# Kernel optimization log

Measured on AMD Instinct MI355X. Metric: run time of the kernel, lower is better.

## Reference

```python
import jax, jax.numpy as jnp
import numpy as np

N = 8192          # number of nodes
DIN = 512         # in_features
DOUT = 256        # out_features
P_EDGE = 0.004    # ~32 avg degree
NEG_INF = -9e15   # matches the torch module's -9000000000000000.0 mask value


def setup_inputs() -> dict:
    key = jax.random.key(0)
    ks = jax.random.split(key, 7)
    x = jax.random.normal(ks[0], (N, DIN), dtype=jnp.float32)
    # binary adjacency, Bernoulli(P_EDGE)
    adj = (jax.random.uniform(ks[1], (N, N)) < P_EDGE).astype(jnp.float32)
    W1 = jax.random.normal(ks[2], (DIN, DOUT), dtype=jnp.float32) * 0.05
    b1 = jnp.zeros((DOUT,), dtype=jnp.float32)
    a1_w = jax.random.normal(ks[3], (DOUT,), dtype=jnp.float32) * 0.05
    a1_b = jnp.zeros((), dtype=jnp.float32)
    a2_w = jax.random.normal(ks[4], (DOUT,), dtype=jnp.float32) * 0.05
    a2_b = jnp.zeros((), dtype=jnp.float32)
    return {"x": x, "adj": adj, "W1": W1, "b1": b1,
            "a1_w": a1_w, "a1_b": a1_b, "a2_w": a2_w, "a2_b": a2_b}


def reference(x, adj, W1, b1, a1_w, a1_b, a2_w, a2_b):
    # h = linear1(elu(x))                       [n, DOUT]
    h = jnp.matmul(jax.nn.elu(x), W1) + b1
    # per-node scalar scores g1 (source/col) and g2 (dest/row)
    g1 = h @ a1_w + a1_b                       # [n]
    g2 = h @ a2_w + a2_b                       # [n]
    # kron trick collapses to: scores[i,j] = adj[i,j] * (g2[i] + g1[j])
    scores = adj * (g2[:, None] + g1[None, :])  # [n, n]
    e = jax.nn.leaky_relu(scores, negative_slope=0.2)
    attention = jax.nn.softmax(jnp.where(adj > 0, e, NEG_INF), axis=1)
    # untied=False path: weighted aggregation of h (dropout p=0 is identity)
    return attention @ h
```

## Files before the change

### kernel.cpp

```cpp
#include <hip/hip_runtime.h>
#include <hip/hip_bf16.h>
#include <cstdint>
#include <cstddef>

#define N_NODES 8192
#define DIN 512
#define DOUT 256
#define CAP 128
#define GEMM_BLKS 512
#define SCAN_BLKS 2048

typedef short bf16x8 __attribute__((ext_vector_type(8)));
typedef float f32x4 __attribute__((ext_vector_type(4)));
typedef unsigned int u32x4 __attribute__((ext_vector_type(4)));

__device__ __forceinline__ float bf2f(unsigned short u) {
    union { unsigned int ui; float f; } v; v.ui = ((unsigned int)u) << 16; return v.f;
}
__device__ __forceinline__ unsigned short f2bf(float f) {
    union { float f; unsigned int u; } v; v.f = f;
    unsigned int u = v.u;
    return (unsigned short)((u + 0x7fffu + ((u >> 16) & 1u)) >> 16);
}
__device__ __forceinline__ float elu1(float v) { return v > 0.f ? v : (expf(v) - 1.f); }

__global__ __launch_bounds__(256) void convw_kernel(
    const float* __restrict__ W1, unsigned short* __restrict__ wb)
{
    const int n = blockIdx.x;
    const int k = threadIdx.x * 2;
    unsigned short a = f2bf(W1[(size_t)k * DOUT + n]);
    unsigned short b = f2bf(W1[(size_t)(k + 1) * DOUT + n]);
    *(unsigned int*)(wb + (size_t)n * DIN + k) = (unsigned int)a | ((unsigned int)b << 16);
}

__global__ __launch_bounds__(256) void fused_kernel(
    const float* __restrict__ x, const unsigned short* __restrict__ wb,
    const float* __restrict__ b1,
    const float* __restrict__ a1w, const float* __restrict__ a1b,
    const float* __restrict__ a2w, const float* __restrict__ a2b,
    unsigned short* __restrict__ h, float* __restrict__ g1, float* __restrict__ g2,
    const float* __restrict__ adj, int* __restrict__ ecnt, int* __restrict__ ecols)
{
    const int tid = threadIdx.x;

    if (blockIdx.x < GEMM_BLKS) {
        const int wave = tid >> 6, lane = tid & 63;
        const int quad = lane >> 4, r16 = lane & 15;
        const int m0 = blockIdx.x * 16;
        const int n0 = wave * 64;

        f32x4 acc[4] = {{0.f,0.f,0.f,0.f},{0.f,0.f,0.f,0.f},{0.f,0.f,0.f,0.f},{0.f,0.f,0.f,0.f}};
        const float* xrow = x + (size_t)(m0 + r16) * DIN;

        for (int k0 = 0; k0 < DIN; k0 += 32) {
            const int kb = k0 + quad * 8;
            float4 f0 = *(const float4*)(xrow + kb);
            float4 f1 = *(const float4*)(xrow + kb + 4);
            bf16x8 A;
            A[0] = (short)f2bf(elu1(f0.x)); A[1] = (short)f2bf(elu1(f0.y));
            A[2] = (short)f2bf(elu1(f0.z)); A[3] = (short)f2bf(elu1(f0.w));
            A[4] = (short)f2bf(elu1(f1.x)); A[5] = (short)f2bf(elu1(f1.y));
            A[6] = (short)f2bf(elu1(f1.z)); A[7] = (short)f2bf(elu1(f1.w));
            bf16x8 B[4];
            #pragma unroll
            for (int s = 0; s < 4; ++s)
                B[s] = *(const bf16x8*)(wb + (size_t)(n0 + s * 16 + r16) * DIN + kb);
            #pragma unroll
            for (int ni = 0; ni < 4; ++ni)
                acc[ni] = __builtin_amdgcn_mfma_f32_16x16x32_bf16(A, B[ni], acc[ni], 0, 0, 0);
        }

        float p1[4] = {0.f, 0.f, 0.f, 0.f};
        float p2[4] = {0.f, 0.f, 0.f, 0.f};
        #pragma unroll
        for (int ni = 0; ni < 4; ++ni) {
            const int col = n0 + ni * 16 + r16;
            const float bias = b1[col];
            const float w1c = a1w[col], w2c = a2w[col];
            #pragma unroll
            for (int rr = 0; rr < 4; ++rr) {
                float val = acc[ni][rr] + bias;
                h[(size_t)(m0 + quad * 4 + rr) * DOUT + col] = f2bf(val);
                p1[rr] += val * w1c;
                p2[rr] += val * w2c;
            }
        }
        #pragma unroll
        for (int off = 1; off < 16; off <<= 1) {
            #pragma unroll
            for (int rr = 0; rr < 4; ++rr) {
                p1[rr] += __shfl_xor(p1[rr], off, 64);
                p2[rr] += __shfl_xor(p2[rr], off, 64);
            }
        }
        __shared__ float sg1[16][4];
        __shared__ float sg2[16][4];
        if (r16 == 0) {
            #pragma unroll
            for (int rr = 0; rr < 4; ++rr) {
                sg1[quad * 4 + rr][wave] = p1[rr];
                sg2[quad * 4 + rr][wave] = p2[rr];
            }
        }
        __syncthreads();
        if (tid < 16) {
            float t1 = sg1[tid][0] + sg1[tid][1] + sg1[tid][2] + sg1[tid][3];
            float t2 = sg2[tid][0] + sg2[tid][1] + sg2[tid][2] + sg2[tid][3];
            g1[m0 + tid] = t1 + a1b[0];
            g2[m0 + tid] = t2 + a2b[0];
        }
        return;
    }

    __shared__ int eidx[4][CAP];
    __shared__ int wcnt[4];

    const int w    = tid >> 6;
    const int lane = tid & 63;
    const int i    = (blockIdx.x - GEMM_BLKS) * 4 + w;

    if (lane == 0) wcnt[w] = 0;

    const float* arow = adj + (size_t)i * N_NODES;

    #pragma unroll 1
    for (int g = 0; g < 4; ++g) {
        u32x4 raws[8];
        #pragma unroll
        for (int c = 0; c < 8; ++c)
            raws[c] = __builtin_nontemporal_load(
                (const u32x4*)(arow + (g * 8 + c) * 256 + lane * 4));
        #pragma unroll
        for (int c = 0; c < 8; ++c) {
            u32x4 raw = raws[c];
            if (raw.x | raw.y | raw.z | raw.w) {
                unsigned int wv[4] = {raw.x, raw.y, raw.z, raw.w};
                #pragma unroll
                for (int q = 0; q < 4; ++q) {
                    if (wv[q]) {
                        int j = (g * 8 + c) * 256 + lane * 4 + q;
                        int pos = atomicAdd(&wcnt[w], 1);
                        if (pos < CAP) eidx[w][pos] = j;
                    }
                }
            }
        }
    }

    int K = wcnt[w];
    if (K > CAP) K = CAP;
    if (lane == 0) ecnt[i] = K;
    for (int k = lane; k < K; k += 64)
        ecols[(size_t)i * CAP + k] = eidx[w][k];
}

__global__ __launch_bounds__(256) void agg2_kernel(
    const int* __restrict__ ecnt, const int* __restrict__ ecols,
    const unsigned short* __restrict__ h,
    const float* __restrict__ g1, const float* __restrict__ g2,
    float* __restrict__ out)
{
    __shared__ float evs[4][CAP];
    __shared__ int   jls[4][CAP];

    const int tid  = threadIdx.x;
    const int w    = tid >> 6;
    const int lane = tid & 63;
    const int i    = blockIdx.x * 4 + w;

    int K = ecnt[i];
    if (K > CAP) K = CAP;
    const float g2i = g2[i];

    if (K == 0) {
        f32x4 acc = {0.f, 0.f, 0.f, 0.f};
        for (int j = 0; j < N_NODES; ++j) {
            ushort4 hv = *(const ushort4*)(h + (size_t)j * DOUT + lane * 4);
            acc[0] += bf2f(hv.x); acc[1] += bf2f(hv.y);
            acc[2] += bf2f(hv.z); acc[3] += bf2f(hv.w);
        }
        const float sc = 1.f / (float)N_NODES;
        float4 o = {acc[0] * sc, acc[1] * sc, acc[2] * sc, acc[3] * sc};
        *(float4*)(out + (size_t)i * DOUT + lane * 4) = o;
        return;
    }

    float e0 = -1e30f, e1 = -1e30f;
    int   j0 = 0,      j1 = 0;
    if (lane < K) {
        j0 = ecols[(size_t)i * CAP + lane];
        float s = g2i + g1[j0];
        e0 = s > 0.f ? s : 0.2f * s;
    }
    if (lane + 64 < K) {
        j1 = ecols[(size_t)i * CAP + lane + 64];
        float s = g2i + g1[j1];
        e1 = s > 0.f ? s : 0.2f * s;
    }
    float m = fmaxf(e0, e1);
    #pragma unroll
    for (int off = 32; off > 0; off >>= 1) m = fmaxf(m, __shfl_xor(m, off, 64));

    float p0 = expf(e0 - m);
    float p1 = expf(e1 - m);
    float ssum = p0 + p1;
    #pragma unroll
    for (int off = 32; off > 0; off >>= 1) ssum += __shfl_xor(ssum, off, 64);
    const float inv = 1.f / ssum;

    evs[w][lane] = p0;      jls[w][lane] = j0;
    evs[w][lane + 64] = p1; jls[w][lane + 64] = j1;

    const unsigned short* hp = h + lane * 4;
    f32x4 accA = {0.f, 0.f, 0.f, 0.f};
    f32x4 accB = {0.f, 0.f, 0.f, 0.f};
    int k = 0;
    for (; k + 4 <= K; k += 4) {
        float q0 = evs[w][k],   q1 = evs[w][k+1], q2 = evs[w][k+2], q3 = evs[w][k+3];
        int   i0 = jls[w][k],   i1 = jls[w][k+1], i2 = jls[w][k+2], i3 = jls[w][k+3];
        ushort4 h0 = *(const ushort4*)(hp + (size_t)i0 * DOUT);
        ushort4 h1 = *(const ushort4*)(hp + (size_t)i1 * DOUT);
        ushort4 h2 = *(const ushort4*)(hp + (size_t)i2 * DOUT);
        ushort4 h3 = *(const ushort4*)(hp + (size_t)i3 * DOUT);
        accA[0] += q0 * bf2f(h0.x); accA[1] += q0 * bf2f(h0.y);
        accA[2] += q0 * bf2f(h0.z); accA[3] += q0 * bf2f(h0.w);
        accB[0] += q1 * bf2f(h1.x); accB[1] += q1 * bf2f(h1.y);
        accB[2] += q1 * bf2f(h1.z); accB[3] += q1 * bf2f(h1.w);
        accA[0] += q2 * bf2f(h2.x); accA[1] += q2 * bf2f(h2.y);
        accA[2] += q2 * bf2f(h2.z); accA[3] += q2 * bf2f(h2.w);
        accB[0] += q3 * bf2f(h3.x); accB[1] += q3 * bf2f(h3.y);
        accB[2] += q3 * bf2f(h3.z); accB[3] += q3 * bf2f(h3.w);
    }
    for (; k < K; ++k) {
        float q = evs[w][k];
        ushort4 hv = *(const ushort4*)(hp + (size_t)jls[w][k] * DOUT);
        accA[0] += q * bf2f(hv.x); accA[1] += q * bf2f(hv.y);
        accA[2] += q * bf2f(hv.z); accA[3] += q * bf2f(hv.w);
    }
    float4 o = {(accA[0] + accB[0]) * inv, (accA[1] + accB[1]) * inv,
                (accA[2] + accB[2]) * inv, (accA[3] + accB[3]) * inv};
    *(float4*)(out + (size_t)i * DOUT + lane * 4) = o;
}

extern "C" void kernel_launch(void* const* d_in, const int* in_sizes, int n_in,
                              void* d_out, int out_size, void* d_ws, size_t ws_size,
                              hipStream_t stream) {
    const float* x   = (const float*)d_in[0];
    const float* adj = (const float*)d_in[1];
    const float* W1  = (const float*)d_in[2];
    const float* b1  = (const float*)d_in[3];
    const float* a1w = (const float*)d_in[4];
    const float* a1b = (const float*)d_in[5];
    const float* a2w = (const float*)d_in[6];
    const float* a2b = (const float*)d_in[7];

    char* w = (char*)d_ws;
    float* g1 = (float*)w;                     w += (size_t)N_NODES * 4;
    float* g2 = (float*)w;                     w += (size_t)N_NODES * 4;
    unsigned short* h  = (unsigned short*)w;   w += (size_t)N_NODES * DOUT * 2;
    unsigned short* wb = (unsigned short*)w;   w += (size_t)DOUT * DIN * 2;
    int* ecnt = (int*)w;                       w += (size_t)N_NODES * 4;
    int* ecols = (int*)w;
    float* out = (float*)d_out;

    hipLaunchKernelGGL(convw_kernel, dim3(256), dim3(256), 0, stream, W1, wb);
    hipLaunchKernelGGL(fused_kernel, dim3(GEMM_BLKS + SCAN_BLKS), dim3(256), 0, stream,
                       x, wb, b1, a1w, a1b, a2w, a2b, h, g1, g2, adj, ecnt, ecols);
    hipLaunchKernelGGL(agg2_kernel, dim3(2048), dim3(256), 0, stream, ecnt, ecols, h, g1, g2, out);
}
```

Measured before the change: 390.6 us.

## Fuse aggregation into scan kernel using a global done-counter spin wait

Merges the aggregation kernel into the fused GEMM+scan kernel. Scan blocks keep their edge lists in shared memory and spin on a global atomic counter until all GEMM blocks have published h, g1 and g2, then compute the softmax and aggregation directly. This removes the ecnt/ecols round-trip through global memory and one kernel launch. In exchange it relies on the GEMM blocks being scheduled before the scan blocks can starve them. It also has a bounded spin that, if it times out, silently reads incomplete data.

```diff
diff --git a/kernel.cpp b/kernel.cpp
--- a/kernel.cpp
+++ b/kernel.cpp
@@ -25,13 +25,14 @@
 __device__ __forceinline__ float elu1(float v) { return v > 0.f ? v : (expf(v) - 1.f); }
 
 __global__ __launch_bounds__(256) void convw_kernel(
-    const float* __restrict__ W1, unsigned short* __restrict__ wb)
+    const float* __restrict__ W1, unsigned short* __restrict__ wb, int* __restrict__ done)
 {
     const int n = blockIdx.x;
     const int k = threadIdx.x * 2;
     unsigned short a = f2bf(W1[(size_t)k * DOUT + n]);
     unsigned short b = f2bf(W1[(size_t)(k + 1) * DOUT + n]);
     *(unsigned int*)(wb + (size_t)n * DIN + k) = (unsigned int)a | ((unsigned int)b << 16);
+    if (blockIdx.x == 0 && threadIdx.x == 0) *done = 0;
 }
 
 __global__ __launch_bounds__(256) void fused_kernel(
@@ -40,7 +41,8 @@
     const float* __restrict__ a1w, const float* __restrict__ a1b,
     const float* __restrict__ a2w, const float* __restrict__ a2b,
     unsigned short* __restrict__ h, float* __restrict__ g1, float* __restrict__ g2,
-    const float* __restrict__ adj, int* __restrict__ ecnt, int* __restrict__ ecols)
+    const float* __restrict__ adj, int* __restrict__ done,
+    float* __restrict__ out)
 {
     const int tid = threadIdx.x;
 
@@ -110,11 +112,15 @@
             g1[m0 + tid] = t1 + a1b[0];
             g2[m0 + tid] = t2 + a2b[0];
         }
+        __syncthreads();
+        if (tid == 0)
+            __hip_atomic_fetch_add(done, 1, __ATOMIC_RELEASE, __HIP_MEMORY_SCOPE_AGENT);
         return;
     }
 
-    __shared__ int eidx[4][CAP];
-    __shared__ int wcnt[4];
+    __shared__ int   eidx[4][CAP];
+    __shared__ float evs[4][CAP];
+    __shared__ int   wcnt[4];
 
     const int w    = tid >> 6;
     const int lane = tid & 63;
@@ -148,28 +154,17 @@
         }
     }
 
+    __syncthreads();
+    if (tid == 0) {
+        int it = 0;
+        while (__hip_atomic_load(done, __ATOMIC_ACQUIRE, __HIP_MEMORY_SCOPE_AGENT) < GEMM_BLKS) {
+            if (++it > (1 << 18)) break;
+            __builtin_amdgcn_s_sleep(2);
+        }
+    }
+    __syncthreads();
+
     int K = wcnt[w];
-    if (K > CAP) K = CAP;
-    if (lane == 0) ecnt[i] = K;
-    for (int k = lane; k < K; k += 64)
-        ecols[(size_t)i * CAP + k] = eidx[w][k];
-}
-
-__global__ __launch_bounds__(256) void agg2_kernel(
-    const int* __restrict__ ecnt, const int* __restrict__ ecols,
-    const unsigned short* __restrict__ h,
-    const float* __restrict__ g1, const float* __restrict__ g2,
-    float* __restrict__ out)
-{
-    __shared__ float evs[4][CAP];
-    __shared__ int   jls[4][CAP];
-
-    const int tid  = threadIdx.x;
-    const int w    = tid >> 6;
-    const int lane = tid & 63;
-    const int i    = blockIdx.x * 4 + w;
-
-    int K = ecnt[i];
     if (K > CAP) K = CAP;
     const float g2i = g2[i];
 
@@ -189,12 +184,12 @@
     float e0 = -1e30f, e1 = -1e30f;
     int   j0 = 0,      j1 = 0;
     if (lane < K) {
-        j0 = ecols[(size_t)i * CAP + lane];
+        j0 = eidx[w][lane];
         float s = g2i + g1[j0];
         e0 = s > 0.f ? s : 0.2f * s;
     }
     if (lane + 64 < K) {
-        j1 = ecols[(size_t)i * CAP + lane + 64];
+        j1 = eidx[w][lane + 64];
         float s = g2i + g1[j1];
         e1 = s > 0.f ? s : 0.2f * s;
     }
@@ -209,8 +204,8 @@
     for (int off = 32; off > 0; off >>= 1) ssum += __shfl_xor(ssum, off, 64);
     const float inv = 1.f / ssum;
 
-    evs[w][lane] = p0;      jls[w][lane] = j0;
-    evs[w][lane + 64] = p1; jls[w][lane + 64] = j1;
+    evs[w][lane] = p0;
+    evs[w][lane + 64] = p1;
 
     const unsigned short* hp = h + lane * 4;
     f32x4 accA = {0.f, 0.f, 0.f, 0.f};
@@ -218,7 +213,7 @@
     int k = 0;
     for (; k + 4 <= K; k += 4) {
         float q0 = evs[w][k],   q1 = evs[w][k+1], q2 = evs[w][k+2], q3 = evs[w][k+3];
-        int   i0 = jls[w][k],   i1 = jls[w][k+1], i2 = jls[w][k+2], i3 = jls[w][k+3];
+        int   i0 = eidx[w][k],  i1 = eidx[w][k+1], i2 = eidx[w][k+2], i3 = eidx[w][k+3];
         ushort4 h0 = *(const ushort4*)(hp + (size_t)i0 * DOUT);
         ushort4 h1 = *(const ushort4*)(hp + (size_t)i1 * DOUT);
         ushort4 h2 = *(const ushort4*)(hp + (size_t)i2 * DOUT);
@@ -234,7 +229,7 @@
     }
     for (; k < K; ++k) {
         float q = evs[w][k];
-        ushort4 hv = *(const ushort4*)(hp + (size_t)jls[w][k] * DOUT);
+        ushort4 hv = *(const ushort4*)(hp + (size_t)eidx[w][k] * DOUT);
         accA[0] += q * bf2f(hv.x); accA[1] += q * bf2f(hv.y);
         accA[2] += q * bf2f(hv.z); accA[3] += q * bf2f(hv.w);
     }
@@ -260,12 +255,10 @@
     float* g2 = (float*)w;                     w += (size_t)N_NODES * 4;
     unsigned short* h  = (unsigned short*)w;   w += (size_t)N_NODES * DOUT * 2;
     unsigned short* wb = (unsigned short*)w;   w += (size_t)DOUT * DIN * 2;
-    int* ecnt = (int*)w;                       w += (size_t)N_NODES * 4;
-    int* ecols = (int*)w;
+    int* done = (int*)w;
     float* out = (float*)d_out;
 
-    hipLaunchKernelGGL(convw_kernel, dim3(256), dim3(256), 0, stream, W1, wb);
+    hipLaunchKernelGGL(convw_kernel, dim3(256), dim3(256), 0, stream, W1, wb, done);
     hipLaunchKernelGGL(fused_kernel, dim3(GEMM_BLKS + SCAN_BLKS), dim3(256), 0, stream,
-                       x, wb, b1, a1w, a1b, a2w, a2b, h, g1, g2, adj, ecnt, ecols);
-    hipLaunchKernelGGL(agg2_kernel, dim3(2048), dim3(256), 0, stream, ecnt, ecols, h, g1, g2, out);
-}
+                       x, wb, b1, a1w, a1b, a2w, a2b, h, g1, g2, adj, done, out);
+}
```

After: 467.2 us. 1.2x slower.
